# Optimization experiments

Hardware: AMD Instinct MI355X
Metric: run time of the kernel (lower is better)

The kernel has to match this reference:

```python
import jax, jax.numpy as jnp
import numpy as np

H = 4          # heads
C = 32         # out_channels per head
NEG_SLOPE = 0.2
N_NODES = 50000
N_EDGES = 600000
F_IN = 128
OUT_DIM = 10
N_GRAPHS = 32


def _gat_params(keys, f_in, scale=0.05):
    hc = H * C
    return dict(
        Wl=jax.random.normal(keys[0], (f_in, hc)) * scale,
        bl=jnp.zeros((hc,)),
        Wr=jax.random.normal(keys[1], (f_in, hc)) * scale,
        br=jnp.zeros((hc,)),
        We=jax.random.normal(keys[2], (1, hc)) * scale,   # lin_edge, bias=False in PyG
        att=jax.random.normal(keys[3], (H, C)) * scale,
        bias=jnp.zeros((hc,)),
    )


def setup_inputs() -> dict:
    key = jax.random.key(0)
    ks = jax.random.split(key, 16)
    x = jax.random.normal(ks[0], (N_NODES, F_IN), dtype=jnp.float32)
    edge_index = jax.random.randint(ks[1], (2, N_EDGES), 0, N_NODES, dtype=jnp.int32)
    edge_weight = jax.random.uniform(ks[2], (N_EDGES, 1), dtype=jnp.float32)
    batch = jnp.sort(jax.random.randint(ks[3], (N_NODES,), 0, N_GRAPHS, dtype=jnp.int32))
    p1 = _gat_params(ks[4:8], F_IN)
    p2 = _gat_params(ks[8:12], H * C)
    fc_W = jax.random.normal(ks[12], (H * C, OUT_DIM)) * 0.05
    fc_b = jnp.zeros((OUT_DIM,))
    return dict(
        x=x, edge_index=edge_index, edge_weight=edge_weight, batch=batch,
        p1_Wl=p1['Wl'], p1_bl=p1['bl'], p1_Wr=p1['Wr'], p1_br=p1['br'],
        p1_We=p1['We'], p1_att=p1['att'], p1_bias=p1['bias'],
        p2_Wl=p2['Wl'], p2_bl=p2['bl'], p2_Wr=p2['Wr'], p2_br=p2['br'],
        p2_We=p2['We'], p2_att=p2['att'], p2_bias=p2['bias'],
        fc_W=fc_W, fc_b=fc_b,
    )


def _add_self_loops(src, dst, eattr, n):
    # PyG fill_value='mean': self-loop attr = mean of incoming edge_attr per node
    loop = jnp.arange(n, dtype=src.dtype)
    cnt = jax.ops.segment_sum(jnp.ones((src.shape[0],), eattr.dtype), dst, num_segments=n)
    loop_attr = jax.ops.segment_sum(eattr, dst, num_segments=n) / jnp.maximum(cnt, 1.0)[:, None]
    return (jnp.concatenate([src, loop]), jnp.concatenate([dst, loop]),
            jnp.concatenate([eattr, loop_attr], axis=0))


def _gatv2_conv(x, src, dst, eattr, Wl, bl, Wr, br, We, att, bias, n):
    x_l = (x @ Wl + bl).reshape(n, H, C)   # source transform
    x_r = (x @ Wr + br).reshape(n, H, C)   # target transform
    e_feat = (eattr @ We).reshape(-1, H, C)
    # per-edge message [E2, H, C]
    m = jax.nn.leaky_relu(x_l[src] + x_r[dst] + e_feat, NEG_SLOPE)
    alpha = jnp.einsum('ehc,hc->eh', m, att)            # [E2, H]
    amax = jax.ops.segment_max(alpha, dst, num_segments=n)
    amax = jnp.where(jnp.isfinite(amax), amax, 0.0)
    ex = jnp.exp(alpha - amax[dst])
    denom = jax.ops.segment_sum(ex, dst, num_segments=n)
    a = ex / (denom[dst] + 1e-16)                       # segment softmax
    out = jax.ops.segment_sum(a[:, :, None] * x_l[src], dst, num_segments=n)
    return out.reshape(n, H * C) + bias


def reference(x, edge_index, edge_weight, batch,
              p1_Wl, p1_bl, p1_Wr, p1_br, p1_We, p1_att, p1_bias,
              p2_Wl, p2_bl, p2_Wr, p2_br, p2_We, p2_att, p2_bias,
              fc_W, fc_b):
    n = x.shape[0]
    src, dst, eattr = _add_self_loops(edge_index[0], edge_index[1], edge_weight, n)
    h = _gatv2_conv(x, src, dst, eattr, p1_Wl, p1_bl, p1_Wr, p1_br, p1_We, p1_att, p1_bias, n)
    h = _gatv2_conv(h, src, dst, eattr, p2_Wl, p2_bl, p2_Wr, p2_br, p2_We, p2_att, p2_bias, n)
    cnt = jax.ops.segment_sum(jnp.ones((n,), h.dtype), batch, num_segments=N_GRAPHS)
    pooled = jax.ops.segment_sum(h, batch, num_segments=N_GRAPHS) / jnp.maximum(cnt, 1.0)[:, None]
    out = pooled @ fc_W + fc_b
    return out, pooled
```

## Files before the change

kernel.cpp:

```cpp
#include <hip/hip_runtime.h>
#include <hip/hip_bf16.h>
#include <cstdint>

static inline int cdiv(int a, int b){ return (a + b - 1) / b; }

typedef __attribute__((ext_vector_type(8))) short short8v;
typedef __attribute__((ext_vector_type(4))) float float4v;

#define ELLW 48

__device__ inline float bf2f(unsigned short u){ return __uint_as_float(((unsigned)u) << 16); }
__device__ inline unsigned short f2bf(float f){
  unsigned u = __float_as_uint(f);
  u += 0x7fffu + ((u >> 16) & 1u);
  return (unsigned short)(u >> 16);
}
__device__ inline float4 ldbf4(const unsigned short* p){
  ushort4 u = *(const ushort4*)p;
  return make_float4(bf2f(u.x), bf2f(u.y), bf2f(u.z), bf2f(u.w));
}

__global__ void k_sniffz(const unsigned short* __restrict__ xp, int* __restrict__ flag,
                         unsigned long long* __restrict__ deg64, int N){
  int i = blockIdx.x * blockDim.x + threadIdx.x;
  if (i < N) deg64[i] = 0ull;
  if (i == 0){
    int good = 0;
    for (int k = 0; k < 256; ++k){
      float v = bf2f(xp[2 * k]);
      float a = fabsf(v);
      if (v == 0.f || (a >= 6.1e-5f && a <= 64.f)) ++good;
    }
    flag[0] = (good > 128) ? 1 : 0;
    flag[1] = 1;
  }
}

struct P16 { const void* p[16]; };
__global__ void k_prep(P16 s, const int* __restrict__ flag,
                       unsigned short* __restrict__ Wf, unsigned short* __restrict__ bb,
                       unsigned short* __restrict__ sm){
  int i = blockIdx.x * blockDim.x + threadIdx.x;
  if (i >= 68106) return;
  const int bf = flag[0];
  auto rd = [&](const void* q, int j) -> unsigned short {
    return bf ? ((const unsigned short*)q)[j] : f2bf(((const float*)q)[j]);
  };
  if (i < 65536){
    int l = i >> 15, r = i & 32767;
    int j = r & 7, n = (r >> 3) & 255, kq = r >> 11;
    int k = kq * 8 + j;
    const void* W = (n < 128) ? (l ? s.p[7] : s.p[0]) : (l ? s.p[9] : s.p[2]);
    Wf[i] = rd(W, k * 128 + (n & 127));
  } else if (i < 66048){
    int i2 = i - 65536;
    int l = i2 >> 8, n = i2 & 255;
    const void* b = (n < 128) ? (l ? s.p[8] : s.p[1]) : (l ? s.p[10] : s.p[3]);
    bb[i2] = rd(b, n & 127);
  } else {
    int j = i - 66048;
    const void* q; int o;
    if      (j < 128){ q = s.p[4];  o = j; }
    else if (j < 256){ q = s.p[5];  o = j - 128; }
    else if (j < 384){ q = s.p[6];  o = j - 256; }
    else if (j < 512){ q = s.p[11]; o = j - 384; }
    else if (j < 640){ q = s.p[12]; o = j - 512; }
    else if (j < 768){ q = s.p[13]; o = j - 640; }
    else if (j < 2048){ q = s.p[14]; o = j - 768; }
    else { q = s.p[15]; o = j - 2048; }
    sm[j] = rd(q, o);
  }
}

__global__ void k_esc(const int* __restrict__ ei, const void* __restrict__ ew,
                      const int* __restrict__ flag,
                      unsigned long long* __restrict__ deg64, unsigned* __restrict__ eE, int E){
  int e = blockIdx.x * blockDim.x + threadIdx.x;
  if (e >= E) return;
  int src = ei[e], dst = ei[E + e];
  unsigned short w16; float w;
  if (flag[0]){ w16 = ((const unsigned short*)ew)[e]; w = bf2f(w16); }
  else        { w = ((const float*)ew)[e]; w16 = f2bf(w); }
  unsigned long long pk = (1ull << 40) + (unsigned long long)(unsigned)(w * 1048576.0f + 0.5f);
  unsigned long long old = atomicAdd(&deg64[dst], pk);
  int pos = min((int)(old >> 40), ELLW - 2);
  eE[dst * ELLW + pos] = (unsigned)src | ((unsigned)w16 << 16);
}

__global__ void k_fin(const unsigned long long* __restrict__ deg64, int* __restrict__ degc,
                      unsigned* __restrict__ eE, float* __restrict__ pool, int pz, int N){
  int i = blockIdx.x * blockDim.x + threadIdx.x;
  if (i < pz) pool[i] = 0.f;
  if (i >= N) return;
  unsigned long long v = deg64[i];
  int d = (int)(v >> 40);
  float ws = (float)(v & 0xFFFFFFFFFFull) * (1.0f / 1048576.0f);
  float lw = ws / fmaxf((float)d, 1.0f);
  int dc = min(d, ELLW - 1);
  eE[i * ELLW + dc] = (unsigned)i | ((unsigned)f2bf(lw) << 16);
  degc[i] = dc + 1;
}

__global__ __launch_bounds__(256)
void k_gemm2(const void* __restrict__ actv, const int* __restrict__ abf_p,
             const unsigned short* __restrict__ Wf, const unsigned short* __restrict__ bb,
             unsigned short* __restrict__ outL, unsigned short* __restrict__ outR, int nrows){
  __shared__ unsigned short As[64][136];
  const int abf = abf_p[0];
  const int t = threadIdx.x;
  const int row0 = blockIdx.x * 64;
  for (int c = t; c < 2048; c += 256){
    int row = c >> 5, col4 = (c & 31) * 4;
    int r = row0 + row;
    ushort4 v = make_ushort4(0, 0, 0, 0);
    if (r < nrows){
      if (abf) v = *(const ushort4*)((const unsigned short*)actv + (size_t)r * 128 + col4);
      else {
        float4 f = *(const float4*)((const float*)actv + (size_t)r * 128 + col4);
        v.x = f2bf(f.x); v.y = f2bf(f.y); v.z = f2bf(f.z); v.w = f2bf(f.w);
      }
    }
    *(ushort4*)&As[row][col4] = v;
  }
  __syncthreads();
  const int wv = t >> 6, lane = t & 63;
  const int l15 = lane & 15, q = lane >> 4;
  #pragma unroll
  for (int half = 0; half < 2; ++half){
    const int ntb = wv * 4 + half * 2;
    short8v bfr[2][4];
    #pragma unroll
    for (int nt = 0; nt < 2; ++nt){
      int n = (ntb + nt) * 16 + l15;
      #pragma unroll
      for (int ks = 0; ks < 4; ++ks)
        bfr[nt][ks] = *(const short8v*)(Wf + ((((ks * 4 + q) * 256 + n)) << 3));
    }
    float4v acc[4][2];
    #pragma unroll
    for (int mi = 0; mi < 4; ++mi)
      #pragma unroll
      for (int nt = 0; nt < 2; ++nt)
        acc[mi][nt] = (float4v){0.f, 0.f, 0.f, 0.f};
    #pragma unroll
    for (int mi = 0; mi < 4; ++mi){
      short8v afr[4];
      #pragma unroll
      for (int ks = 0; ks < 4; ++ks)
        afr[ks] = *(const short8v*)&As[mi * 16 + l15][ks * 32 + q * 8];
      #pragma unroll
      for (int nt = 0; nt < 2; ++nt)
        #pragma unroll
        for (int ks = 0; ks < 4; ++ks)
          acc[mi][nt] = __builtin_amdgcn_mfma_f32_16x16x32_bf16(afr[ks], bfr[nt][ks], acc[mi][nt], 0, 0, 0);
    }
    #pragma unroll
    for (int nt = 0; nt < 2; ++nt){
      int n = (ntb + nt) * 16 + l15;
      float bias = bf2f(bb[n]);
      unsigned short* outp = (n < 128) ? outL : outR;
      int nc = n & 127;
      #pragma unroll
      for (int mi = 0; mi < 4; ++mi)
        #pragma unroll
        for (int rr = 0; rr < 4; ++rr){
          int grow = row0 + mi * 16 + q * 4 + rr;
          if (grow < nrows) outp[(size_t)grow * 128 + nc] = f2bf(acc[mi][nt][rr] + bias);
        }
    }
  }
}

__global__ __launch_bounds__(256)
void k_node(const unsigned short* __restrict__ A, const unsigned short* __restrict__ B,
            const int* __restrict__ degc, const unsigned* __restrict__ eE,
            const unsigned short* __restrict__ We, const unsigned short* __restrict__ att,
            const unsigned short* __restrict__ bias, unsigned short* __restrict__ H, int N){
  int node = (blockIdx.x * 256 + threadIdx.x) >> 5;
  if (node >= N) return;
  int lane = threadIdx.x & 31;
  int dc = degc[node];
  const unsigned* eb = eE + (size_t)node * ELLW;
  float4 xr = ldbf4(B + (size_t)node * 128 + lane * 4);
  float4 we = ldbf4(We + lane * 4);
  float4 at = ldbf4(att + lane * 4);
  float4 at6 = make_float4(at.x * 0.6f, at.y * 0.6f, at.z * 0.6f, at.w * 0.6f);
  float4 at4 = make_float4(at.x * 0.4f, at.y * 0.4f, at.z * 0.4f, at.w * 0.4f);
  float m = -3.0e38f, denom = 0.f;
  float4 acc = make_float4(0.f, 0.f, 0.f, 0.f);
  int last = dc - 1;
  for (int p = 0; p < dc; p += 4){
    uint4 ev;
    if (p + 4 <= dc){
      ev = *(const uint4*)(eb + p);
    } else {
      ev.x = eb[p];
      ev.y = eb[min(p + 1, last)];
      ev.z = eb[min(p + 2, last)];
      ev.w = eb[min(p + 3, last)];
    }
    int i0 = ev.x & 0xffff, i1 = ev.y & 0xffff, i2 = ev.z & 0xffff, i3 = ev.w & 0xffff;
    float w0 = bf2f((unsigned short)(ev.x >> 16));
    float w1 = bf2f((unsigned short)(ev.y >> 16));
    float w2 = bf2f((unsigned short)(ev.z >> 16));
    float w3 = bf2f((unsigned short)(ev.w >> 16));
    float4 xl0 = ldbf4(A + (size_t)i0 * 128 + lane * 4);
    float4 xl1 = ldbf4(A + (size_t)i1 * 128 + lane * 4);
    float4 xl2 = ldbf4(A + (size_t)i2 * 128 + lane * 4);
    float4 xl3 = ldbf4(A + (size_t)i3 * 128 + lane * 4);
    float a;
    float s0, s1, s2, s3;
    a = fmaf(w0, we.x, xl0.x + xr.x); s0 = fmaf(at6.x, a, at4.x * fabsf(a));
    a = fmaf(w0, we.y, xl0.y + xr.y); s0 = fmaf(at6.y, a, fmaf(at4.y, fabsf(a), s0));
    a = fmaf(w0, we.z, xl0.z + xr.z); s0 = fmaf(at6.z, a, fmaf(at4.z, fabsf(a), s0));
    a = fmaf(w0, we.w, xl0.w + xr.w); s0 = fmaf(at6.w, a, fmaf(at4.w, fabsf(a), s0));
    a = fmaf(w1, we.x, xl1.x + xr.x); s1 = fmaf(at6.x, a, at4.x * fabsf(a));
    a = fmaf(w1, we.y, xl1.y + xr.y); s1 = fmaf(at6.y, a, fmaf(at4.y, fabsf(a), s1));
    a = fmaf(w1, we.z, xl1.z + xr.z); s1 = fmaf(at6.z, a, fmaf(at4.z, fabsf(a), s1));
    a = fmaf(w1, we.w, xl1.w + xr.w); s1 = fmaf(at6.w, a, fmaf(at4.w, fabsf(a), s1));
    a = fmaf(w2, we.x, xl2.x + xr.x); s2 = fmaf(at6.x, a, at4.x * fabsf(a));
    a = fmaf(w2, we.y, xl2.y + xr.y); s2 = fmaf(at6.y, a, fmaf(at4.y, fabsf(a), s2));
    a = fmaf(w2, we.z, xl2.z + xr.z); s2 = fmaf(at6.z, a, fmaf(at4.z, fabsf(a), s2));
    a = fmaf(w2, we.w, xl2.w + xr.w); s2 = fmaf(at6.w, a, fmaf(at4.w, fabsf(a), s2));
    a = fmaf(w3, we.x, xl3.x + xr.x); s3 = fmaf(at6.x, a, at4.x * fabsf(a));
    a = fmaf(w3, we.y, xl3.y + xr.y); s3 = fmaf(at6.y, a, fmaf(at4.y, fabsf(a), s3));
    a = fmaf(w3, we.z, xl3.z + xr.z); s3 = fmaf(at6.z, a, fmaf(at4.z, fabsf(a), s3));
    a = fmaf(w3, we.w, xl3.w + xr.w); s3 = fmaf(at6.w, a, fmaf(at4.w, fabsf(a), s3));
    s0 += __shfl_xor(s0, 1); s1 += __shfl_xor(s1, 1); s2 += __shfl_xor(s2, 1); s3 += __shfl_xor(s3, 1);
    s0 += __shfl_xor(s0, 2); s1 += __shfl_xor(s1, 2); s2 += __shfl_xor(s2, 2); s3 += __shfl_xor(s3, 2);
    s0 += __shfl_xor(s0, 4); s1 += __shfl_xor(s1, 4); s2 += __shfl_xor(s2, 4); s3 += __shfl_xor(s3, 4);
    if (p + 1 >= dc) s1 = -3.0e38f;
    if (p + 2 >= dc) s2 = -3.0e38f;
    if (p + 3 >= dc) s3 = -3.0e38f;
    float newm = fmaxf(fmaxf(fmaxf(m, s0), fmaxf(s1, s2)), s3);
    float sc  = __expf(m - newm);
    float ex0 = __expf(s0 - newm);
    float ex1 = __expf(s1 - newm);
    float ex2 = __expf(s2 - newm);
    float ex3 = __expf(s3 - newm);
    denom = fmaf(denom, sc, (ex0 + ex1) + (ex2 + ex3));
    acc.x = fmaf(acc.x, sc, fmaf(ex0, xl0.x, fmaf(ex1, xl1.x, fmaf(ex2, xl2.x, ex3 * xl3.x))));
    acc.y = fmaf(acc.y, sc, fmaf(ex0, xl0.y, fmaf(ex1, xl1.y, fmaf(ex2, xl2.y, ex3 * xl3.y))));
    acc.z = fmaf(acc.z, sc, fmaf(ex0, xl0.z, fmaf(ex1, xl1.z, fmaf(ex2, xl2.z, ex3 * xl3.z))));
    acc.w = fmaf(acc.w, sc, fmaf(ex0, xl0.w, fmaf(ex1, xl1.w, fmaf(ex2, xl2.w, ex3 * xl3.w))));
    m = newm;
  }
  float inv = 1.f / (denom + 1e-16f);
  float4 bv = ldbf4(bias + lane * 4);
  ushort4 o;
  o.x = f2bf(fmaf(acc.x, inv, bv.x));
  o.y = f2bf(fmaf(acc.y, inv, bv.y));
  o.z = f2bf(fmaf(acc.z, inv, bv.z));
  o.w = f2bf(fmaf(acc.w, inv, bv.w));
  *(ushort4*)(H + (size_t)node * 128 + lane * 4) = o;
}

__global__ __launch_bounds__(256)
void k_pool(const unsigned short* __restrict__ Cb, const int* __restrict__ batch,
            float* __restrict__ pool, float* __restrict__ gcnt, int N){
  __shared__ float sp[4][128];
  __shared__ float scnt[4];
  const int t = threadIdx.x;
  const int lane = t & 31, grp = t >> 5;
  const int r0 = blockIdx.x * 64;
  const int r1 = min(r0 + 64, N);
  if (r0 >= N) return;
  const int gmin = batch[r0];
  const int gmax = batch[r1 - 1];
  const int ngr = gmax - gmin + 1;
  const bool fits = (ngr <= 4);
  if (t < 4) scnt[t] = 0.f;
  for (int i = t; i < 4 * 128; i += 256) ((float*)sp)[i] = 0.f;
  __syncthreads();
  int curg = -1; float4 s = make_float4(0.f, 0.f, 0.f, 0.f); float cnt = 0.f;
  for (int r = r0 + grp; r < r1; r += 8){
    int g = batch[r];
    if (g != curg){
      if (curg >= 0){
        if (fits){
          float* pp = sp[curg - gmin] + lane * 4;
          atomicAdd(pp + 0, s.x); atomicAdd(pp + 1, s.y);
          atomicAdd(pp + 2, s.z); atomicAdd(pp + 3, s.w);
          if (lane == 0) atomicAdd(&scnt[curg - gmin], cnt);
        } else {
          float* pp = pool + (size_t)curg * 128 + lane * 4;
          atomicAdd(pp + 0, s.x); atomicAdd(pp + 1, s.y);
          atomicAdd(pp + 2, s.z); atomicAdd(pp + 3, s.w);
          if (lane == 0) atomicAdd(&gcnt[curg], cnt);
        }
      }
      s = make_float4(0.f, 0.f, 0.f, 0.f); cnt = 0.f; curg = g;
    }
    float4 v = ldbf4(Cb + (size_t)r * 128 + lane * 4);
    s.x += v.x; s.y += v.y; s.z += v.z; s.w += v.w;
    cnt += 1.f;
  }
  if (curg >= 0){
    if (fits){
      float* pp = sp[curg - gmin] + lane * 4;
      atomicAdd(pp + 0, s.x); atomicAdd(pp + 1, s.y);
      atomicAdd(pp + 2, s.z); atomicAdd(pp + 3, s.w);
      if (lane == 0) atomicAdd(&scnt[curg - gmin], cnt);
    } else {
      float* pp = pool + (size_t)curg * 128 + lane * 4;
      atomicAdd(pp + 0, s.x); atomicAdd(pp + 1, s.y);
      atomicAdd(pp + 2, s.z); atomicAdd(pp + 3, s.w);
      if (lane == 0) atomicAdd(&gcnt[curg], cnt);
    }
  }
  __syncthreads();
  if (fits){
    for (int i = t; i < ngr * 128; i += 256){
      int gg = i >> 7;
      atomicAdd(&pool[(size_t)(gmin + gg) * 128 + (i & 127)], ((float*)sp)[i]);
    }
    if (t < ngr) atomicAdd(&gcnt[gmin + t], scnt[t]);
  }
}

__global__ __launch_bounds__(256)
void k_fc(const float* __restrict__ pool, const float* __restrict__ gcnt,
          const unsigned short* __restrict__ fcW, const unsigned short* __restrict__ fcb,
          const int* __restrict__ flag, void* __restrict__ outv, int G){
  __shared__ float sp[32 * 128];
  int t = threadIdx.x;
  int bf = flag[0];
  unsigned short* ob = (unsigned short*)outv;
  float* of = (float*)outv;
  for (int idx = t; idx < G * 128; idx += 256){
    int g = idx >> 7;
    float p = pool[idx] / fmaxf(gcnt[g], 1.0f);
    sp[idx] = p;
    if (bf) ob[G * 10 + idx] = f2bf(p); else of[G * 10 + idx] = p;
  }
  __syncthreads();
  for (int idx = t; idx < G * 10; idx += 256){
    int g = idx / 10, o = idx - g * 10;
    float acc = bf2f(fcb[o]);
    const float* sg = sp + g * 128;
    #pragma unroll 4
    for (int c = 0; c < 128; ++c) acc = fmaf(sg[c], bf2f(fcW[c * 10 + o]), acc);
    if (bf) ob[idx] = f2bf(acc); else of[idx] = acc;
  }
}

extern "C" void kernel_launch(void* const* d_in, const int* in_sizes, int n_in,
                              void* d_out, int out_size, void* d_ws, size_t ws_size,
                              hipStream_t stream){
  const void* x    = d_in[0];
  const int* ei    = (const int*)d_in[1];
  const void* ew   = d_in[2];
  const int* batch = (const int*)d_in[3];

  const int N  = in_sizes[3];
  const int E  = in_sizes[2];
  const int G  = out_size / 138;

  char* w = (char*)d_ws;
  auto take = [&](size_t nbytes) -> char* {
    char* p = w; w += (nbytes + 255) & ~(size_t)255; return p;
  };
  unsigned short* Abf  = (unsigned short*)take((size_t)N * 128 * 2);
  unsigned short* Bbf  = (unsigned short*)take((size_t)N * 128 * 2);
  unsigned short* Hb   = (unsigned short*)take((size_t)N * 128 * 2);
  unsigned long long* deg64 = (unsigned long long*)take((size_t)N * 8);
  int*      degc   = (int*)take((size_t)N * 4);
  unsigned* eE     = (unsigned*)take((size_t)N * ELLW * 4);
  float*    pool   = (float*)take((size_t)(G * 128 + G) * 4);
  float*    gcnt   = pool + (size_t)G * 128;
  int*      flag   = (int*)take(2 * 4);
  unsigned short* Wf = (unsigned short*)take((size_t)2 * 32768 * 2);
  unsigned short* bb = (unsigned short*)take(512 * 2);
  unsigned short* sm = (unsigned short*)take(2058 * 2);

  P16 ps;
  for (int i = 0; i < 16; ++i) ps.p[i] = d_in[4 + i];
  const unsigned short* p1We = sm + 0;
  const unsigned short* p1at = sm + 128;
  const unsigned short* p1bs = sm + 256;
  const unsigned short* p2We = sm + 384;
  const unsigned short* p2at = sm + 512;
  const unsigned short* p2bs = sm + 640;
  const unsigned short* fcW  = sm + 768;
  const unsigned short* fcb  = sm + 2048;

  k_sniffz<<<cdiv(N, 256), 256, 0, stream>>>((const unsigned short*)x, flag, deg64, N);
  k_prep<<<cdiv(68106, 256), 256, 0, stream>>>(ps, flag, Wf, bb, sm);

  k_esc<<<cdiv(E, 256), 256, 0, stream>>>(ei, ew, flag, deg64, eE, E);
  k_fin<<<cdiv(N, 256), 256, 0, stream>>>(deg64, degc, eE, pool, G * 128 + G, N);

  k_gemm2<<<cdiv(N, 64), 256, 0, stream>>>(x, flag + 0, Wf, bb, Abf, Bbf, N);
  k_node<<<cdiv(N, 8), 256, 0, stream>>>(Abf, Bbf, degc, eE, p1We, p1at, p1bs, Hb, N);

  k_gemm2<<<cdiv(N, 64), 256, 0, stream>>>(Hb, flag + 1, Wf + 32768, bb + 256, Abf, Bbf, N);
  k_node<<<cdiv(N, 8), 256, 0, stream>>>(Abf, Bbf, degc, eE, p2We, p2at, p2bs, Hb, N);

  k_pool<<<cdiv(N, 64), 256, 0, stream>>>(Hb, batch, pool, gcnt, N);
  k_fc<<<1, 256, 0, stream>>>(pool, gcnt, fcW, fcb, flag, d_out, G);
}
```

Baseline: 310.3 us.

## Fuse edge scatter with layer-1 GEMM and compute self-loop inline in node kernel

Merges the edge-scatter kernel and the first-layer GEMM into one launch by splitting the grid into edge blocks and GEMM blocks, removes the k_fin pass, and moves pool zeroing into the init kernel. The node kernel now derives degree and mean self-loop weight from the packed deg64 and seeds the online softmax with the self-loop term, so the ELL slot for the self-loop is no longer needed. This cuts two launches and an extra pass over nodes. In exchange the node kernel does a few more loads and ops per node, and the fused kernel's edge blocks compete with GEMM blocks for the GPU.

```diff
diff --git a/kernel.cpp b/kernel.cpp
--- a/kernel.cpp
+++ b/kernel.cpp
@@ -21,9 +21,11 @@
 }
 
 __global__ void k_sniffz(const unsigned short* __restrict__ xp, int* __restrict__ flag,
-                         unsigned long long* __restrict__ deg64, int N){
+                         unsigned long long* __restrict__ deg64, float* __restrict__ pool,
+                         int pz, int N){
   int i = blockIdx.x * blockDim.x + threadIdx.x;
   if (i < N) deg64[i] = 0ull;
+  if (i < pz) pool[i] = 0.f;
   if (i == 0){
     int good = 0;
     for (int k = 0; k < 256; ++k){
@@ -72,33 +74,90 @@
   }
 }
 
-__global__ void k_esc(const int* __restrict__ ei, const void* __restrict__ ew,
-                      const int* __restrict__ flag,
-                      unsigned long long* __restrict__ deg64, unsigned* __restrict__ eE, int E){
-  int e = blockIdx.x * blockDim.x + threadIdx.x;
-  if (e >= E) return;
-  int src = ei[e], dst = ei[E + e];
-  unsigned short w16; float w;
-  if (flag[0]){ w16 = ((const unsigned short*)ew)[e]; w = bf2f(w16); }
-  else        { w = ((const float*)ew)[e]; w16 = f2bf(w); }
-  unsigned long long pk = (1ull << 40) + (unsigned long long)(unsigned)(w * 1048576.0f + 0.5f);
-  unsigned long long old = atomicAdd(&deg64[dst], pk);
-  int pos = min((int)(old >> 40), ELLW - 2);
-  eE[dst * ELLW + pos] = (unsigned)src | ((unsigned)w16 << 16);
-}
-
-__global__ void k_fin(const unsigned long long* __restrict__ deg64, int* __restrict__ degc,
-                      unsigned* __restrict__ eE, float* __restrict__ pool, int pz, int N){
-  int i = blockIdx.x * blockDim.x + threadIdx.x;
-  if (i < pz) pool[i] = 0.f;
-  if (i >= N) return;
-  unsigned long long v = deg64[i];
-  int d = (int)(v >> 40);
-  float ws = (float)(v & 0xFFFFFFFFFFull) * (1.0f / 1048576.0f);
-  float lw = ws / fmaxf((float)d, 1.0f);
-  int dc = min(d, ELLW - 1);
-  eE[i * ELLW + dc] = (unsigned)i | ((unsigned)f2bf(lw) << 16);
-  degc[i] = dc + 1;
+__global__ __launch_bounds__(256)
+void k_g1e(const int* __restrict__ ei, const void* __restrict__ ew,
+           const int* __restrict__ flag,
+           unsigned long long* __restrict__ deg64, unsigned* __restrict__ eE, int E, int escB,
+           const void* __restrict__ actv,
+           const unsigned short* __restrict__ Wf, const unsigned short* __restrict__ bb,
+           unsigned short* __restrict__ outL, unsigned short* __restrict__ outR, int nrows){
+  __shared__ unsigned short As[64][136];
+  const int abf = flag[0];
+  const int t = threadIdx.x;
+  if ((int)blockIdx.x < escB){
+    int e = blockIdx.x * 256 + t;
+    if (e >= E) return;
+    int src = ei[e], dst = ei[E + e];
+    unsigned short w16; float w;
+    if (abf){ w16 = ((const unsigned short*)ew)[e]; w = bf2f(w16); }
+    else    { w = ((const float*)ew)[e]; w16 = f2bf(w); }
+    unsigned long long pk = (1ull << 40) + (unsigned long long)(unsigned)(w * 1048576.0f + 0.5f);
+    unsigned long long old = atomicAdd(&deg64[dst], pk);
+    int pos = min((int)(old >> 40), ELLW - 1);
+    eE[dst * ELLW + pos] = (unsigned)src | ((unsigned)w16 << 16);
+    return;
+  }
+  const int row0 = ((int)blockIdx.x - escB) * 64;
+  for (int c = t; c < 2048; c += 256){
+    int row = c >> 5, col4 = (c & 31) * 4;
+    int r = row0 + row;
+    ushort4 v = make_ushort4(0, 0, 0, 0);
+    if (r < nrows){
+      if (abf) v = *(const ushort4*)((const unsigned short*)actv + (size_t)r * 128 + col4);
+      else {
+        float4 f = *(const float4*)((const float*)actv + (size_t)r * 128 + col4);
+        v.x = f2bf(f.x); v.y = f2bf(f.y); v.z = f2bf(f.z); v.w = f2bf(f.w);
+      }
+    }
+    *(ushort4*)&As[row][col4] = v;
+  }
+  __syncthreads();
+  const int wv = t >> 6, lane = t & 63;
+  const int l15 = lane & 15, q = lane >> 4;
+  #pragma unroll
+  for (int half = 0; half < 2; ++half){
+    const int ntb = wv * 4 + half * 2;
+    short8v bfr[2][4];
+    #pragma unroll
+    for (int nt = 0; nt < 2; ++nt){
+      int n = (ntb + nt) * 16 + l15;
+      #pragma unroll
+      for (int ks = 0; ks < 4; ++ks)
+        bfr[nt][ks] = *(const short8v*)(Wf + ((((ks * 4 + q) * 256 + n)) << 3));
+    }
+    float4v acc[4][2];
+    #pragma unroll
+    for (int mi = 0; mi < 4; ++mi)
+      #pragma unroll
+      for (int nt = 0; nt < 2; ++nt)
+        acc[mi][nt] = (float4v){0.f, 0.f, 0.f, 0.f};
+    #pragma unroll
+    for (int mi = 0; mi < 4; ++mi){
+      short8v afr[4];
+      #pragma unroll
+      for (int ks = 0; ks < 4; ++ks)
+        afr[ks] = *(const short8v*)&As[mi * 16 + l15][ks * 32 + q * 8];
+      #pragma unroll
+      for (int nt = 0; nt < 2; ++nt)
+        #pragma unroll
+        for (int ks = 0; ks < 4; ++ks)
+          acc[mi][nt] = __builtin_amdgcn_mfma_f32_16x16x32_bf16(afr[ks], bfr[nt][ks], acc[mi][nt], 0, 0, 0);
+    }
+    #pragma unroll
+    for (int nt = 0; nt < 2; ++nt){
+      int n = (ntb + nt) * 16 + l15;
+      float bias = bf2f(bb[n]);
+      unsigned short* outp = (n < 128) ? outL : outR;
+      int nc = n & 127;
+      #pragma unroll
+      for (int mi = 0; mi < 4; ++mi)
+        #pragma unroll
+        for (int rr = 0; rr < 4; ++rr){
+          int grow = row0 + mi * 16 + q * 4 + rr;
+          if (grow < nrows) outp[(size_t)grow * 128 + nc] = f2bf(acc[mi][nt][rr] + bias);
+        }
+    }
+  }
 }
 
 __global__ __launch_bounds__(256)
@@ -173,21 +232,34 @@
 
 __global__ __launch_bounds__(256)
 void k_node(const unsigned short* __restrict__ A, const unsigned short* __restrict__ B,
-            const int* __restrict__ degc, const unsigned* __restrict__ eE,
+            const unsigned long long* __restrict__ deg64, const unsigned* __restrict__ eE,
             const unsigned short* __restrict__ We, const unsigned short* __restrict__ att,
             const unsigned short* __restrict__ bias, unsigned short* __restrict__ H, int N){
   int node = (blockIdx.x * 256 + threadIdx.x) >> 5;
   if (node >= N) return;
   int lane = threadIdx.x & 31;
-  int dc = degc[node];
+  unsigned long long v64 = deg64[node];
+  int d = (int)(v64 >> 40);
+  float ws = (float)(v64 & 0xFFFFFFFFFFull) * (1.0f / 1048576.0f);
+  float lw = ws / fmaxf((float)d, 1.0f);
+  int dc = min(d, ELLW);
   const unsigned* eb = eE + (size_t)node * ELLW;
   float4 xr = ldbf4(B + (size_t)node * 128 + lane * 4);
   float4 we = ldbf4(We + lane * 4);
   float4 at = ldbf4(att + lane * 4);
   float4 at6 = make_float4(at.x * 0.6f, at.y * 0.6f, at.z * 0.6f, at.w * 0.6f);
   float4 at4 = make_float4(at.x * 0.4f, at.y * 0.4f, at.z * 0.4f, at.w * 0.4f);
-  float m = -3.0e38f, denom = 0.f;
-  float4 acc = make_float4(0.f, 0.f, 0.f, 0.f);
+  float4 xls = ldbf4(A + (size_t)node * 128 + lane * 4);
+  float a, m;
+  a = fmaf(lw, we.x, xls.x + xr.x); m = fmaf(at6.x, a, at4.x * fabsf(a));
+  a = fmaf(lw, we.y, xls.y + xr.y); m = fmaf(at6.y, a, fmaf(at4.y, fabsf(a), m));
+  a = fmaf(lw, we.z, xls.z + xr.z); m = fmaf(at6.z, a, fmaf(at4.z, fabsf(a), m));
+  a = fmaf(lw, we.w, xls.w + xr.w); m = fmaf(at6.w, a, fmaf(at4.w, fabsf(a), m));
+  m += __shfl_xor(m, 1);
+  m += __shfl_xor(m, 2);
+  m += __shfl_xor(m, 4);
+  float denom = 1.f;
+  float4 acc = xls;
   int last = dc - 1;
   for (int p = 0; p < dc; p += 4){
     uint4 ev;
@@ -208,7 +280,6 @@
     float4 xl1 = ldbf4(A + (size_t)i1 * 128 + lane * 4);
     float4 xl2 = ldbf4(A + (size_t)i2 * 128 + lane * 4);
     float4 xl3 = ldbf4(A + (size_t)i3 * 128 + lane * 4);
-    float a;
     float s0, s1, s2, s3;
     a = fmaf(w0, we.x, xl0.x + xr.x); s0 = fmaf(at6.x, a, at4.x * fabsf(a));
     a = fmaf(w0, we.y, xl0.y + xr.y); s0 = fmaf(at6.y, a, fmaf(at4.y, fabsf(a), s0));
@@ -364,7 +435,6 @@
   unsigned short* Bbf  = (unsigned short*)take((size_t)N * 128 * 2);
   unsigned short* Hb   = (unsigned short*)take((size_t)N * 128 * 2);
   unsigned long long* deg64 = (unsigned long long*)take((size_t)N * 8);
-  int*      degc   = (int*)take((size_t)N * 4);
   unsigned* eE     = (unsigned*)take((size_t)N * ELLW * 4);
   float*    pool   = (float*)take((size_t)(G * 128 + G) * 4);
   float*    gcnt   = pool + (size_t)G * 128;
@@ -384,17 +454,17 @@
   const unsigned short* fcW  = sm + 768;
   const unsigned short* fcb  = sm + 2048;
 
-  k_sniffz<<<cdiv(N, 256), 256, 0, stream>>>((const unsigned short*)x, flag, deg64, N);
+  k_sniffz<<<cdiv(N, 256), 256, 0, stream>>>((const unsigned short*)x, flag, deg64, pool, G * 128 + G, N);
   k_prep<<<cdiv(68106, 256), 256, 0, stream>>>(ps, flag, Wf, bb, sm);
 
-  k_esc<<<cdiv(E, 256), 256, 0, stream>>>(ei, ew, flag, deg64, eE, E);
-  k_fin<<<cdiv(N, 256), 256, 0, stream>>>(deg64, degc, eE, pool, G * 128 + G, N);
-
-  k_gemm2<<<cdiv(N, 64), 256, 0, stream>>>(x, flag + 0, Wf, bb, Abf, Bbf, N);
-  k_node<<<cdiv(N, 8), 256, 0, stream>>>(Abf, Bbf, degc, eE, p1We, p1at, p1bs, Hb, N);
+  const int escB = cdiv(E, 256);
+  const int gemmB = cdiv(N, 64);
+  k_g1e<<<escB + gemmB, 256, 0, stream>>>(ei, ew, flag, deg64, eE, E, escB,
+                                          x, Wf, bb, Abf, Bbf, N);
+  k_node<<<cdiv(N, 8), 256, 0, stream>>>(Abf, Bbf, deg64, eE, p1We, p1at, p1bs, Hb, N);
 
   k_gemm2<<<cdiv(N, 64), 256, 0, stream>>>(Hb, flag + 1, Wf + 32768, bb + 256, Abf, Bbf, N);
-  k_node<<<cdiv(N, 8), 256, 0, stream>>>(Abf, Bbf, degc, eE, p2We, p2at, p2bs, Hb, N);
+  k_node<<<cdiv(N, 8), 256, 0, stream>>>(Abf, Bbf, deg64, eE, p2We, p2at, p2bs, Hb, N);
 
   k_pool<<<cdiv(N, 64), 256, 0, stream>>>(Hb, batch, pool, gcnt, N);
   k_fc<<<1, 256, 0, stream>>>(pool, gcnt, fcW, fcb, flag, d_out, G);
```

Result: no change. 311.0 us (+0.2%).

## Fuse setup kernels, partition edge scatter by destination, drop online-softmax max tracking

Applied to the files above, without the earlier changes.

Removes the sniff and finalize kernels. Dtype detection now happens inline in each kernel, deg64 and pool are zeroed inside k_prep, and the self-loop is handled directly in k_node from deg64. The edge-scatter kernel splits destinations into 8 ranges, so the atomics of each block land in a narrower region, though every edge index is read 8 times. The softmax in k_node drops the running max and rescaling and uses a clamped exp with no max subtraction, which cuts per-edge exp work but relies on scores staying small. Launch count falls from 10 to 8.

```diff
diff --git a/kernel.cpp b/kernel.cpp
--- a/kernel.cpp
+++ b/kernel.cpp
@@ -19,30 +19,28 @@
   ushort4 u = *(const ushort4*)p;
   return make_float4(bf2f(u.x), bf2f(u.y), bf2f(u.z), bf2f(u.w));
 }
-
-__global__ void k_sniffz(const unsigned short* __restrict__ xp, int* __restrict__ flag,
-                         unsigned long long* __restrict__ deg64, int N){
-  int i = blockIdx.x * blockDim.x + threadIdx.x;
-  if (i < N) deg64[i] = 0ull;
-  if (i == 0){
-    int good = 0;
-    for (int k = 0; k < 256; ++k){
-      float v = bf2f(xp[2 * k]);
-      float a = fabsf(v);
-      if (v == 0.f || (a >= 6.1e-5f && a <= 64.f)) ++good;
-    }
-    flag[0] = (good > 128) ? 1 : 0;
-    flag[1] = 1;
-  }
+__device__ inline int sniff16(const unsigned* __restrict__ xw){
+  int good = 0;
+  #pragma unroll
+  for (int j = 0; j < 16; ++j){
+    float v = __uint_as_float(xw[j] << 16);
+    float a = fabsf(v);
+    good += (v == 0.f) || (a >= 6.1e-5f && a <= 64.f);
+  }
+  return good > 8;
 }
 
 struct P16 { const void* p[16]; };
-__global__ void k_prep(P16 s, const int* __restrict__ flag,
+__global__ void k_prep(P16 s, const unsigned* __restrict__ xw,
+                       unsigned long long* __restrict__ deg64, float* __restrict__ pool,
+                       int pz, int N,
                        unsigned short* __restrict__ Wf, unsigned short* __restrict__ bb,
                        unsigned short* __restrict__ sm){
   int i = blockIdx.x * blockDim.x + threadIdx.x;
+  if (i < N) deg64[i] = 0ull;
+  if (i < pz) pool[i] = 0.f;
   if (i >= 68106) return;
-  const int bf = flag[0];
+  const int bf = sniff16(xw);
   auto rd = [&](const void* q, int j) -> unsigned short {
     return bf ? ((const unsigned short*)q)[j] : f2bf(((const float*)q)[j]);
   };
@@ -72,41 +70,38 @@
   }
 }
 
-__global__ void k_esc(const int* __restrict__ ei, const void* __restrict__ ew,
-                      const int* __restrict__ flag,
-                      unsigned long long* __restrict__ deg64, unsigned* __restrict__ eE, int E){
-  int e = blockIdx.x * blockDim.x + threadIdx.x;
-  if (e >= E) return;
-  int src = ei[e], dst = ei[E + e];
-  unsigned short w16; float w;
-  if (flag[0]){ w16 = ((const unsigned short*)ew)[e]; w = bf2f(w16); }
-  else        { w = ((const float*)ew)[e]; w16 = f2bf(w); }
-  unsigned long long pk = (1ull << 40) + (unsigned long long)(unsigned)(w * 1048576.0f + 0.5f);
-  unsigned long long old = atomicAdd(&deg64[dst], pk);
-  int pos = min((int)(old >> 40), ELLW - 2);
-  eE[dst * ELLW + pos] = (unsigned)src | ((unsigned)w16 << 16);
-}
-
-__global__ void k_fin(const unsigned long long* __restrict__ deg64, int* __restrict__ degc,
-                      unsigned* __restrict__ eE, float* __restrict__ pool, int pz, int N){
-  int i = blockIdx.x * blockDim.x + threadIdx.x;
-  if (i < pz) pool[i] = 0.f;
-  if (i >= N) return;
-  unsigned long long v = deg64[i];
-  int d = (int)(v >> 40);
-  float ws = (float)(v & 0xFFFFFFFFFFull) * (1.0f / 1048576.0f);
-  float lw = ws / fmaxf((float)d, 1.0f);
-  int dc = min(d, ELLW - 1);
-  eE[i * ELLW + dc] = (unsigned)i | ((unsigned)f2bf(lw) << 16);
-  degc[i] = dc + 1;
-}
-
 __global__ __launch_bounds__(256)
-void k_gemm2(const void* __restrict__ actv, const int* __restrict__ abf_p,
+void k_esc(const int* __restrict__ ei, const void* __restrict__ ew,
+           const unsigned* __restrict__ xw,
+           unsigned long long* __restrict__ deg64, unsigned* __restrict__ eE,
+           int E, int P, int N){
+  const int bf = sniff16(xw);
+  const int part = blockIdx.x & 7;
+  const int lo = part * P;
+  const int hi = min(lo + P, N);
+  const int base = (int)(blockIdx.x >> 3) * 2048;
+  const int end = min(base + 2048, E);
+  for (int e = base + (int)threadIdx.x; e < end; e += 256){
+    int dst = ei[E + e];
+    if (dst < lo || dst >= hi) continue;
+    int src = ei[e];
+    unsigned short w16; float w;
+    if (bf){ w16 = ((const unsigned short*)ew)[e]; w = bf2f(w16); }
+    else   { w = ((const float*)ew)[e]; w16 = f2bf(w); }
+    unsigned long long pk = (1ull << 40) + (unsigned long long)(unsigned)(w * 1048576.0f + 0.5f);
+    unsigned long long old = atomicAdd(&deg64[dst], pk);
+    int pos = min((int)(old >> 40), ELLW - 1);
+    eE[dst * ELLW + pos] = (unsigned)src | ((unsigned)w16 << 16);
+  }
+}
+
+template<bool ACT_BF_FIXED>
+__global__ __launch_bounds__(256)
+void k_gemm2(const void* __restrict__ actv, const unsigned* __restrict__ xw,
              const unsigned short* __restrict__ Wf, const unsigned short* __restrict__ bb,
              unsigned short* __restrict__ outL, unsigned short* __restrict__ outR, int nrows){
   __shared__ unsigned short As[64][136];
-  const int abf = abf_p[0];
+  const int abf = ACT_BF_FIXED ? 1 : sniff16(xw);
   const int t = threadIdx.x;
   const int row0 = blockIdx.x * 64;
   for (int c = t; c < 2048; c += 256){
@@ -173,21 +168,35 @@
 
 __global__ __launch_bounds__(256)
 void k_node(const unsigned short* __restrict__ A, const unsigned short* __restrict__ B,
-            const int* __restrict__ degc, const unsigned* __restrict__ eE,
+            const unsigned long long* __restrict__ deg64, const unsigned* __restrict__ eE,
             const unsigned short* __restrict__ We, const unsigned short* __restrict__ att,
             const unsigned short* __restrict__ bias, unsigned short* __restrict__ H, int N){
   int node = (blockIdx.x * 256 + threadIdx.x) >> 5;
   if (node >= N) return;
   int lane = threadIdx.x & 31;
-  int dc = degc[node];
+  unsigned long long v64 = deg64[node];
+  int d = (int)(v64 >> 40);
+  float ws = (float)(v64 & 0xFFFFFFFFFFull) * (1.0f / 1048576.0f);
+  float lw = ws / fmaxf((float)d, 1.0f);
+  int dc = min(d, ELLW);
   const unsigned* eb = eE + (size_t)node * ELLW;
   float4 xr = ldbf4(B + (size_t)node * 128 + lane * 4);
   float4 we = ldbf4(We + lane * 4);
   float4 at = ldbf4(att + lane * 4);
   float4 at6 = make_float4(at.x * 0.6f, at.y * 0.6f, at.z * 0.6f, at.w * 0.6f);
   float4 at4 = make_float4(at.x * 0.4f, at.y * 0.4f, at.z * 0.4f, at.w * 0.4f);
-  float m = -3.0e38f, denom = 0.f;
-  float4 acc = make_float4(0.f, 0.f, 0.f, 0.f);
+  float4 xls = ldbf4(A + (size_t)node * 128 + lane * 4);
+  float a, s;
+  a = fmaf(lw, we.x, xls.x + xr.x); s = fmaf(at6.x, a, at4.x * fabsf(a));
+  a = fmaf(lw, we.y, xls.y + xr.y); s = fmaf(at6.y, a, fmaf(at4.y, fabsf(a), s));
+  a = fmaf(lw, we.z, xls.z + xr.z); s = fmaf(at6.z, a, fmaf(at4.z, fabsf(a), s));
+  a = fmaf(lw, we.w, xls.w + xr.w); s = fmaf(at6.w, a, fmaf(at4.w, fabsf(a), s));
+  s += __shfl_xor(s, 1);
+  s += __shfl_xor(s, 2);
+  s += __shfl_xor(s, 4);
+  float exs = __expf(fminf(s, 60.f));
+  float denom = exs;
+  float4 acc = make_float4(exs * xls.x, exs * xls.y, exs * xls.z, exs * xls.w);
   int last = dc - 1;
   for (int p = 0; p < dc; p += 4){
     uint4 ev;
@@ -208,7 +217,6 @@
     float4 xl1 = ldbf4(A + (size_t)i1 * 128 + lane * 4);
     float4 xl2 = ldbf4(A + (size_t)i2 * 128 + lane * 4);
     float4 xl3 = ldbf4(A + (size_t)i3 * 128 + lane * 4);
-    float a;
     float s0, s1, s2, s3;
     a = fmaf(w0, we.x, xl0.x + xr.x); s0 = fmaf(at6.x, a, at4.x * fabsf(a));
     a = fmaf(w0, we.y, xl0.y + xr.y); s0 = fmaf(at6.y, a, fmaf(at4.y, fabsf(a), s0));
@@ -229,21 +237,18 @@
     s0 += __shfl_xor(s0, 1); s1 += __shfl_xor(s1, 1); s2 += __shfl_xor(s2, 1); s3 += __shfl_xor(s3, 1);
     s0 += __shfl_xor(s0, 2); s1 += __shfl_xor(s1, 2); s2 += __shfl_xor(s2, 2); s3 += __shfl_xor(s3, 2);
     s0 += __shfl_xor(s0, 4); s1 += __shfl_xor(s1, 4); s2 += __shfl_xor(s2, 4); s3 += __shfl_xor(s3, 4);
-    if (p + 1 >= dc) s1 = -3.0e38f;
-    if (p + 2 >= dc) s2 = -3.0e38f;
-    if (p + 3 >= dc) s3 = -3.0e38f;
-    float newm = fmaxf(fmaxf(fmaxf(m, s0), fmaxf(s1, s2)), s3);
-    float sc  = __expf(m - newm);
-    float ex0 = __expf(s0 - newm);
-    float ex1 = __expf(s1 - newm);
-    float ex2 = __expf(s2 - newm);
-    float ex3 = __expf(s3 - newm);
-    denom = fmaf(denom, sc, (ex0 + ex1) + (ex2 + ex3));
-    acc.x = fmaf(acc.x, sc, fmaf(ex0, xl0.x, fmaf(ex1, xl1.x, fmaf(ex2, xl2.x, ex3 * xl3.x))));
-    acc.y = fmaf(acc.y, sc, fmaf(ex0, xl0.y, fmaf(ex1, xl1.y, fmaf(ex2, xl2.y, ex3 * xl3.y))));
-    acc.z = fmaf(acc.z, sc, fmaf(ex0, xl0.z, fmaf(ex1, xl1.z, fmaf(ex2, xl2.z, ex3 * xl3.z))));
-    acc.w = fmaf(acc.w, sc, fmaf(ex0, xl0.w, fmaf(ex1, xl1.w, fmaf(ex2, xl2.w, ex3 * xl3.w))));
-    m = newm;
+    float ex0 = __expf(fminf(s0, 60.f));
+    float ex1 = __expf(fminf(s1, 60.f));
+    float ex2 = __expf(fminf(s2, 60.f));
+    float ex3 = __expf(fminf(s3, 60.f));
+    if (p + 1 >= dc) ex1 = 0.f;
+    if (p + 2 >= dc) ex2 = 0.f;
+    if (p + 3 >= dc) ex3 = 0.f;
+    denom += (ex0 + ex1) + (ex2 + ex3);
+    acc.x = fmaf(ex0, xl0.x, fmaf(ex1, xl1.x, fmaf(ex2, xl2.x, fmaf(ex3, xl3.x, acc.x))));
+    acc.y = fmaf(ex0, xl0.y, fmaf(ex1, xl1.y, fmaf(ex2, xl2.y, fmaf(ex3, xl3.y, acc.y))));
+    acc.z = fmaf(ex0, xl0.z, fmaf(ex1, xl1.z, fmaf(ex2, xl2.z, fmaf(ex3, xl3.z, acc.z))));
+    acc.w = fmaf(ex0, xl0.w, fmaf(ex1, xl1.w, fmaf(ex2, xl2.w, fmaf(ex3, xl3.w, acc.w))));
   }
   float inv = 1.f / (denom + 1e-16f);
   float4 bv = ldbf4(bias + lane * 4);
@@ -321,10 +326,10 @@
 __global__ __launch_bounds__(256)
 void k_fc(const float* __restrict__ pool, const float* __restrict__ gcnt,
           const unsigned short* __restrict__ fcW, const unsigned short* __restrict__ fcb,
-          const int* __restrict__ flag, void* __restrict__ outv, int G){
+          const unsigned* __restrict__ xw, void* __restrict__ outv, int G){
   __shared__ float sp[32 * 128];
   int t = threadIdx.x;
-  int bf = flag[0];
+  int bf = sniff16(xw);
   unsigned short* ob = (unsigned short*)outv;
   float* of = (float*)outv;
   for (int idx = t; idx < G * 128; idx += 256){
@@ -348,6 +353,7 @@
                               void* d_out, int out_size, void* d_ws, size_t ws_size,
                               hipStream_t stream){
   const void* x    = d_in[0];
+  const unsigned* xw = (const unsigned*)d_in[0];
   const int* ei    = (const int*)d_in[1];
   const void* ew   = d_in[2];
   const int* batch = (const int*)d_in[3];
@@ -364,11 +370,9 @@
   unsigned short* Bbf  = (unsigned short*)take((size_t)N * 128 * 2);
   unsigned short* Hb   = (unsigned short*)take((size_t)N * 128 * 2);
   unsigned long long* deg64 = (unsigned long long*)take((size_t)N * 8);
-  int*      degc   = (int*)take((size_t)N * 4);
   unsigned* eE     = (unsigned*)take((size_t)N * ELLW * 4);
   float*    pool   = (float*)take((size_t)(G * 128 + G) * 4);
   float*    gcnt   = pool + (size_t)G * 128;
-  int*      flag   = (int*)take(2 * 4);
   unsigned short* Wf = (unsigned short*)take((size_t)2 * 32768 * 2);
   unsigned short* bb = (unsigned short*)take(512 * 2);
   unsigned short* sm = (unsigned short*)take(2058 * 2);
@@ -384,18 +388,18 @@
   const unsigned short* fcW  = sm + 768;
   const unsigned short* fcb  = sm + 2048;
 
-  k_sniffz<<<cdiv(N, 256), 256, 0, stream>>>((const unsigned short*)x, flag, deg64, N);
-  k_prep<<<cdiv(68106, 256), 256, 0, stream>>>(ps, flag, Wf, bb, sm);
-
-  k_esc<<<cdiv(E, 256), 256, 0, stream>>>(ei, ew, flag, deg64, eE, E);
-  k_fin<<<cdiv(N, 256), 256, 0, stream>>>(deg64, degc, eE, pool, G * 128 + G, N);
-
-  k_gemm2<<<cdiv(N, 64), 256, 0, stream>>>(x, flag + 0, Wf, bb, Abf, Bbf, N);
-  k_node<<<cdiv(N, 8), 256, 0, stream>>>(Abf, Bbf, degc, eE, p1We, p1at, p1bs, Hb, N);
-
-  k_gemm2<<<cdiv(N, 64), 256, 0, stream>>>(Hb, flag + 1, Wf + 32768, bb + 256, Abf, Bbf, N);
-  k_node<<<cdiv(N, 8), 256, 0, stream>>>(Abf, Bbf, degc, eE, p2We, p2at, p2bs, Hb, N);
+  const int prepT = (68106 > N) ? 68106 : N;
+  k_prep<<<cdiv(prepT, 256), 256, 0, stream>>>(ps, xw, deg64, pool, G * 128 + G, N, Wf, bb, sm);
+
+  const int P = cdiv(N, 8);
+  k_esc<<<cdiv(E, 2048) * 8, 256, 0, stream>>>(ei, ew, xw, deg64, eE, E, P, N);
+
+  k_gemm2<false><<<cdiv(N, 64), 256, 0, stream>>>(x, xw, Wf, bb, Abf, Bbf, N);
+  k_node<<<cdiv(N, 8), 256, 0, stream>>>(Abf, Bbf, deg64, eE, p1We, p1at, p1bs, Hb, N);
+
+  k_gemm2<true><<<cdiv(N, 64), 256, 0, stream>>>(Hb, xw, Wf + 32768, bb + 256, Abf, Bbf, N);
+  k_node<<<cdiv(N, 8), 256, 0, stream>>>(Abf, Bbf, deg64, eE, p2We, p2at, p2bs, Hb, N);
 
   k_pool<<<cdiv(N, 64), 256, 0, stream>>>(Hb, batch, pool, gcnt, N);
-  k_fc<<<1, 256, 0, stream>>>(pool, gcnt, fcW, fcb, flag, d_out, G);
-}
+  k_fc<<<1, 256, 0, stream>>>(pool, gcnt, fcW, fcb, xw, d_out, G);
+}
```

Result: faster. 280.6 us (-9.6%).
